# Optimization experiments

Hardware: AMD Instinct MI355X
Metric: run time of the kernel (lower is better)

## Reference

```python
import jax, jax.numpy as jnp
import numpy as np

B, T, E = 4, 2_000_000, 8
C, K, STRIDE = 128, 512, 512
CHUNK, OVERLAP = 64000, 511  # overlap defaults to kernel_size - 1


def _candidate_positions(T):
    """Exact set of window start positions visited by the chunked streaming max.

    Replays the chunk loop of _lowmem_max_over_time: chunk starts advance by
    step = chunk_size - overlap (not a multiple of stride!), and within each
    chunk conv windows start at chunk_start + stride*k.
    """
    step = max(1, CHUNK - OVERLAP)
    pos = []
    start = 0
    while start < T:
        end = min(start + CHUNK, T)
        end_ext = min(end + OVERLAP, T)
        L = end_ext - start
        if L >= K:
            n = (L - K) // STRIDE + 1
            pos.append(start + STRIDE * np.arange(n, dtype=np.int64))
        if end == T:
            break
        start += step
    p = np.unique(np.concatenate(pos))
    return np.clip(p, 0, max(0, T - K))


POS = _candidate_positions(T)                       # [P] static window starts
WIN_IDX = POS[:, None] + np.arange(K, dtype=np.int64)  # [P, K] gather indices


def setup_inputs() -> dict:
    key = jax.random.key(0)
    ks = jax.random.split(key, 5)
    scale = 1.0 / float(np.sqrt(E * K))  # torch Conv1d default init range
    return {
        "x": jax.random.normal(ks[0], (B, T, E), dtype=jnp.float32),
        "w1": jax.random.uniform(ks[1], (C, E, K), jnp.float32, -scale, scale),
        "b1": jax.random.uniform(ks[2], (C,), jnp.float32, -scale, scale),
        "w2": jax.random.uniform(ks[3], (C, E, K), jnp.float32, -scale, scale),
        "b2": jax.random.uniform(ks[4], (C,), jnp.float32, -scale, scale),
    }


def reference(x, w1, b1, w2, b2):
    # Gather every candidate window the chunked scan would see: [B, P, K, E]
    wins = x[:, WIN_IDX, :]
    # Original clones windows under no_grad (stop_grad_input=True): input gets no grad.
    wins = jax.lax.stop_gradient(wins)
    # Gated conv (GLU): conv1(z) * sigmoid(conv2(z)) at each window -> [B, C, P]
    c1 = jnp.einsum('bpke,cek->bcp', wins, w1) + b1[:, None]
    c2 = jnp.einsum('bpke,cek->bcp', wins, w2) + b2[:, None]
    g = c1 * jax.nn.sigmoid(c2)
    # Global max-over-time per (batch, channel); identical value to the
    # running-max pass followed by exact re-evaluation at argmax positions.
    return g.max(axis=-1)  # [B, C]
```

## Files before the change

### kernel.cpp

```cpp
#include <hip/hip_runtime.h>


#define T_LEN 2000000
#define P_CNT 3937
#define M_TOT 15748
#define KD    4096

typedef __attribute__((ext_vector_type(8))) short short8;
typedef __attribute__((ext_vector_type(4))) float f32x4;

static __device__ __forceinline__ unsigned short f2bf(float f) {
    unsigned u = __builtin_bit_cast(unsigned, f);
    unsigned r = (u + 0x7FFFu + ((u >> 16) & 1u)) >> 16;
    return (unsigned short)r;
}

static __device__ __forceinline__ unsigned ordenc(float f) {
    unsigned u = __builtin_bit_cast(unsigned, f);
    return (u & 0x80000000u) ? ~u : (u | 0x80000000u);
}

static __device__ __forceinline__ size_t row_base(int m) {
    if (m > M_TOT - 1) m = M_TOT - 1;
    int bb = m / P_CNT;
    int p  = m - bb * P_CNT;
    int j, kp;
    if (p < 3875) { j = p / 125; kp = p - j * 125; }
    else          { j = 31;      kp = p - 3875; }
    long pos = (long)j * 63489 + (long)kp * 512;
    return ((size_t)bb * T_LEN + (size_t)pos) * 8u;
}

static __device__ __forceinline__ uint2 cvt4(float4 v) {
    unsigned lo, hi;
    asm("v_cvt_pk_bf16_f32 %0, %1, %2" : "=v"(lo) : "v"(v.x), "v"(v.y));
    asm("v_cvt_pk_bf16_f32 %0, %1, %2" : "=v"(hi) : "v"(v.z), "v"(v.w));
    uint2 u; u.x = lo; u.y = hi;
    return u;
}

__global__ __launch_bounds__(256) void pack_w(const float* __restrict__ w1,
                                              const float* __restrict__ w2,
                                              uint4* __restrict__ Bpf,
                                              unsigned* __restrict__ outu) {
    int c = blockIdx.x * 256 + threadIdx.x;
    if (c < 512) outu[c] = 0u;
    if (c >= 131072) return;
    int l  = c & 63;
    int nt = (c >> 6) & 15;
    int kq = (c >> 10) & 1;
    int ks = c >> 11;
    int n  = nt * 16 + (l & 15);
    int kb = ks * 64 + kq * 32 + ((l >> 4) << 3);
    const float* src = (n < 128) ? w1 : w2;
    int cc = n & 127;
    unsigned short h[8];
#pragma unroll
    for (int j = 0; j < 8; ++j) {
        int k = kb + j;
        h[j] = f2bf(src[cc * 4096 + (k & 7) * 512 + (k >> 3)]);
    }
    uint4 v;
    v.x = (unsigned)h[0] | ((unsigned)h[1] << 16);
    v.y = (unsigned)h[2] | ((unsigned)h[3] << 16);
    v.z = (unsigned)h[4] | ((unsigned)h[5] << 16);
    v.w = (unsigned)h[6] | ((unsigned)h[7] << 16);
    Bpf[c] = v;
}

#define LOAD_B(BB, KS)                                                         \
    do {                                                                       \
        _Pragma("unroll")                                                      \
        for (int kq = 0; kq < 2; ++kq)                                         \
            _Pragma("unroll")                                                  \
            for (int nf = 0; nf < 2; ++nf)                                     \
                BB[kq][nf] = Bq[((KS) * 2 + kq) * 1024 + bbase + nf * 64];     \
    } while (0)

#define STEP(KS, BCUR, BNXT)                                                   \
    do {                                                                       \
        const int ks_ = (KS);                                                  \
        const int ksn = (ks_ + 1 < 64) ? ks_ + 1 : 63;                         \
        LOAD_B(BNXT, ksn);                                \
        const int ksl = (ks_ + 4 < 64) ? ks_ + 4 : 63;                         \
        float4 aF = *(const float4*)(x + aoff + (size_t)(ksl * 64));           \
        const char* As = smem + (ks_ & 3) * 4096;                              \
        _Pragma("unroll")                                                      \
        for (int kq = 0; kq < 2; ++kq) {                                       \
            short8 af0 = *(const short8*)(As + aro[kq][0]);                    \
            short8 af1 = *(const short8*)(As + aro[kq][1]);                    \
            short8 b0  = __builtin_bit_cast(short8, BCUR[kq][0]);              \
            short8 b1  = __builtin_bit_cast(short8, BCUR[kq][1]);              \
            acc[0][0] = __builtin_amdgcn_mfma_f32_16x16x32_bf16(               \
                af0, b0, acc[0][0], 0, 0, 0);                                  \
            acc[1][0] = __builtin_amdgcn_mfma_f32_16x16x32_bf16(               \
                af1, b0, acc[1][0], 0, 0, 0);                                  \
            acc[0][1] = __builtin_amdgcn_mfma_f32_16x16x32_bf16(               \
                af0, b1, acc[0][1], 0, 0, 0);                                  \
            acc[1][1] = __builtin_amdgcn_mfma_f32_16x16x32_bf16(               \
                af1, b1, acc[1][1], 0, 0, 0);                                  \
        }                                                                      \
                  \
        *(uint2*)(smem + ((ks_ + 2) & 3) * 4096 + awb) = cvt4(aA);             \
        aA = aB; aB = aF;                                                      \
        asm volatile("s_waitcnt lgkmcnt(0)" ::: "memory");                     \
        __builtin_amdgcn_s_barrier();                                          \
        asm volatile("" ::: "memory");                                         \
    } while (0)

__global__ __launch_bounds__(512, 4) void gemm_max(const float* __restrict__ x,
                                                   const uint4* __restrict__ Bq,
                                                   const float* __restrict__ b1,
                                                   const float* __restrict__ b2,
                                                   unsigned* __restrict__ outu) {
    __shared__ __align__(16) char smem[32768];

    const int t    = threadIdx.x;
    const int lane = t & 63;
    const int w    = t >> 6;
    const int m0   = blockIdx.x * 32;

    const int rowS = t >> 4;
    const int kcS  = t & 15;
    const size_t aoff = row_base(m0 + rowS) + (size_t)(kcS * 4);
    const int    awb  = (rowS * 128 + kcS * 8) ^ ((rowS & 7) << 4);

    int aro[2][2];
#pragma unroll
    for (int kq = 0; kq < 2; ++kq)
#pragma unroll
        for (int mf = 0; mf < 2; ++mf) {
            int row = mf * 16 + (lane & 15);
            aro[kq][mf] = (row * 128 + kq * 64 + (lane >> 4) * 16)
                          ^ ((row & 7) << 4);
        }

    const int bbase = w * 128 + lane;

#pragma unroll
    for (int pt = 0; pt < 2; ++pt) {
        float4 v = *(const float4*)(x + aoff + pt * 64);
        *(uint2*)(smem + pt * 4096 + awb) = cvt4(v);
    }
    __syncthreads();

    float4 aA = *(const float4*)(x + aoff + 128);
    float4 aB = *(const float4*)(x + aoff + 192);
    uint4 BX[2][2], BY[2][2];
    LOAD_B(BX, 0);

    f32x4 acc[2][2];
#pragma unroll
    for (int mf = 0; mf < 2; ++mf)
#pragma unroll
        for (int nf = 0; nf < 2; ++nf) acc[mf][nf] = (f32x4){0.f, 0.f, 0.f, 0.f};

    for (int ks = 0; ks < 64; ks += 2) {
        STEP(ks, BX, BY);
        STEP(ks + 1, BY, BX);
    }

    float* gt = (float*)smem;
#pragma unroll
    for (int mf = 0; mf < 2; ++mf)
#pragma unroll
        for (int nf = 0; nf < 2; ++nf) {
            int col = w * 32 + nf * 16 + (lane & 15);
#pragma unroll
            for (int q = 0; q < 4; ++q) {
                int row = mf * 16 + (lane >> 4) * 4 + q;
                gt[row * 256 + col] = acc[mf][nf][q];
            }
        }
    __syncthreads();

    if (t < 128) {
        const int   c   = t;
        const float bb1 = b1[c];
        const float bb2 = b2[c];
        int   bprev = (m0 < M_TOT ? m0 : M_TOT - 1) / P_CNT;
        float best  = -3.4e38f;
        for (int r = 0; r < 32; ++r) {
            int m = m0 + r;
            if (m > M_TOT - 1) m = M_TOT - 1;
            int bb = m / P_CNT;
            float c1 = gt[r * 256 + c] + bb1;
            float c2 = gt[r * 256 + 128 + c] + bb2;
            float g  = c1 / (1.f + __expf(-c2));
            if (bb != bprev) {
                atomicMax(&outu[bprev * 128 + c], ordenc(best));
                bprev = bb;
                best  = -3.4e38f;
            }
            best = fmaxf(best, g);
        }
        atomicMax(&outu[bprev * 128 + c], ordenc(best));
    }
}

__global__ __launch_bounds__(256) void unmap_out(unsigned* __restrict__ outu) {
    int i = blockIdx.x * 256 + threadIdx.x;
    if (i < 512) {
        unsigned u = outu[i];
        outu[i] = (u & 0x80000000u) ? (u ^ 0x80000000u) : ~u;
    }
}

extern "C" void kernel_launch(void* const* d_in, const int* in_sizes, int n_in,
                              void* d_out, int out_size, void* d_ws, size_t ws_size,
                              hipStream_t stream) {
    const float* x  = (const float*)d_in[0];
    const float* w1 = (const float*)d_in[1];
    const float* b1 = (const float*)d_in[2];
    const float* w2 = (const float*)d_in[3];
    const float* b2 = (const float*)d_in[4];

    uint4*    Bpf  = (uint4*)d_ws;
    unsigned* outu = (unsigned*)d_out;

    pack_w<<<dim3(512), dim3(256), 0, stream>>>(w1, w2, Bpf, outu);

    const int nblk = (M_TOT + 31) / 32;
    gemm_max<<<dim3(nblk), dim3(512), 0, stream>>>(x, (const uint4*)Bpf, b1, b2, outu);

    unmap_out<<<dim3(2), dim3(256), 0, stream>>>(outu);
}
```

Before: 81.92 us.

## Widen GEMM tile to 64 rows with 16 waves and fuse GLU-max into registers

Each block now covers 64 window rows of one batch using 1024 threads (16 waves). Weight columns are interleaved so every 16-wide MFMA tile holds 8 conv1 and 8 conv2 channels. The gated activation and the max are then computed in registers through lane shuffles, replacing the shared-memory staging and the serial 128-thread epilogue. Blocks are aligned to batch boundaries, so each channel needs a single atomic, and each wave loads half as much B per K step. The cost is a larger block, a 1024-thread launch bound that limits registers per thread, and only 248 blocks.

```diff
diff --git a/kernel.cpp b/kernel.cpp
--- a/kernel.cpp
+++ b/kernel.cpp
@@ -20,10 +20,7 @@
     return (u & 0x80000000u) ? ~u : (u | 0x80000000u);
 }
 
-static __device__ __forceinline__ size_t row_base(int m) {
-    if (m > M_TOT - 1) m = M_TOT - 1;
-    int bb = m / P_CNT;
-    int p  = m - bb * P_CNT;
+static __device__ __forceinline__ size_t row_base_bp(int bb, int p) {
     int j, kp;
     if (p < 3875) { j = p / 125; kp = p - j * 125; }
     else          { j = 31;      kp = p - 3875; }
@@ -47,10 +44,11 @@
     if (c < 512) outu[c] = 0u;
     if (c >= 131072) return;
     int l  = c & 63;
-    int nt = (c >> 6) & 15;
+    int w  = (c >> 6) & 15;
     int kq = (c >> 10) & 1;
     int ks = c >> 11;
-    int n  = nt * 16 + (l & 15);
+    int cl = l & 15;
+    int n  = (cl < 8) ? (w * 8 + cl) : (128 + w * 8 + (cl - 8));
     int kb = ks * 64 + kq * 32 + ((l >> 4) << 3);
     const float* src = (n < 128) ? w1 : w2;
     int cc = n & 127;
@@ -72,130 +70,106 @@
     do {                                                                       \
         _Pragma("unroll")                                                      \
         for (int kq = 0; kq < 2; ++kq)                                         \
-            _Pragma("unroll")                                                  \
-            for (int nf = 0; nf < 2; ++nf)                                     \
-                BB[kq][nf] = Bq[((KS) * 2 + kq) * 1024 + bbase + nf * 64];     \
+            BB[kq] = Bq[((KS) * 2 + kq) * 1024 + bbase];                       \
     } while (0)
 
 #define STEP(KS, BCUR, BNXT)                                                   \
     do {                                                                       \
         const int ks_ = (KS);                                                  \
         const int ksn = (ks_ + 1 < 64) ? ks_ + 1 : 63;                         \
-        LOAD_B(BNXT, ksn);                                \
+        LOAD_B(BNXT, ksn);                                                     \
         const int ksl = (ks_ + 4 < 64) ? ks_ + 4 : 63;                         \
         float4 aF = *(const float4*)(x + aoff + (size_t)(ksl * 64));           \
-        const char* As = smem + (ks_ & 3) * 4096;                              \
+        const char* As = smem + (ks_ & 3) * 8192;                              \
         _Pragma("unroll")                                                      \
         for (int kq = 0; kq < 2; ++kq) {                                       \
-            short8 af0 = *(const short8*)(As + aro[kq][0]);                    \
-            short8 af1 = *(const short8*)(As + aro[kq][1]);                    \
-            short8 b0  = __builtin_bit_cast(short8, BCUR[kq][0]);              \
-            short8 b1  = __builtin_bit_cast(short8, BCUR[kq][1]);              \
-            acc[0][0] = __builtin_amdgcn_mfma_f32_16x16x32_bf16(               \
-                af0, b0, acc[0][0], 0, 0, 0);                                  \
-            acc[1][0] = __builtin_amdgcn_mfma_f32_16x16x32_bf16(               \
-                af1, b0, acc[1][0], 0, 0, 0);                                  \
-            acc[0][1] = __builtin_amdgcn_mfma_f32_16x16x32_bf16(               \
-                af0, b1, acc[0][1], 0, 0, 0);                                  \
-            acc[1][1] = __builtin_amdgcn_mfma_f32_16x16x32_bf16(               \
-                af1, b1, acc[1][1], 0, 0, 0);                                  \
+            short8 b = __builtin_bit_cast(short8, BCUR[kq]);                   \
+            _Pragma("unroll")                                                  \
+            for (int mf = 0; mf < 4; ++mf) {                                   \
+                short8 af = *(const short8*)(As + aro[kq][mf]);                \
+                acc[mf] = __builtin_amdgcn_mfma_f32_16x16x32_bf16(             \
+                    af, b, acc[mf], 0, 0, 0);                                  \
+            }                                                                  \
         }                                                                      \
-                  \
-        *(uint2*)(smem + ((ks_ + 2) & 3) * 4096 + awb) = cvt4(aA);             \
+        *(uint2*)(smem + ((ks_ + 2) & 3) * 8192 + awb) = cvt4(aA);             \
         aA = aB; aB = aF;                                                      \
         asm volatile("s_waitcnt lgkmcnt(0)" ::: "memory");                     \
         __builtin_amdgcn_s_barrier();                                          \
         asm volatile("" ::: "memory");                                         \
     } while (0)
 
-__global__ __launch_bounds__(512, 4) void gemm_max(const float* __restrict__ x,
-                                                   const uint4* __restrict__ Bq,
-                                                   const float* __restrict__ b1,
-                                                   const float* __restrict__ b2,
-                                                   unsigned* __restrict__ outu) {
+__global__ __launch_bounds__(1024, 4) void gemm_max(const float* __restrict__ x,
+                                                    const uint4* __restrict__ Bq,
+                                                    const float* __restrict__ b1,
+                                                    const float* __restrict__ b2,
+                                                    unsigned* __restrict__ outu) {
     __shared__ __align__(16) char smem[32768];
 
     const int t    = threadIdx.x;
     const int lane = t & 63;
     const int w    = t >> 6;
-    const int m0   = blockIdx.x * 32;
+    const int bid  = blockIdx.x;
+    const int bb   = bid / 62;
+    const int p0   = (bid % 62) * 64;
 
     const int rowS = t >> 4;
     const int kcS  = t & 15;
-    const size_t aoff = row_base(m0 + rowS) + (size_t)(kcS * 4);
+    int pS = p0 + rowS; if (pS > P_CNT - 1) pS = P_CNT - 1;
+    const size_t aoff = row_base_bp(bb, pS) + (size_t)(kcS * 4);
     const int    awb  = (rowS * 128 + kcS * 8) ^ ((rowS & 7) << 4);
 
-    int aro[2][2];
+    int aro[2][2 * 2];
 #pragma unroll
     for (int kq = 0; kq < 2; ++kq)
 #pragma unroll
-        for (int mf = 0; mf < 2; ++mf) {
+        for (int mf = 0; mf < 4; ++mf) {
             int row = mf * 16 + (lane & 15);
             aro[kq][mf] = (row * 128 + kq * 64 + (lane >> 4) * 16)
                           ^ ((row & 7) << 4);
         }
 
-    const int bbase = w * 128 + lane;
+    const int bbase = w * 64 + lane;
 
 #pragma unroll
     for (int pt = 0; pt < 2; ++pt) {
         float4 v = *(const float4*)(x + aoff + pt * 64);
-        *(uint2*)(smem + pt * 4096 + awb) = cvt4(v);
+        *(uint2*)(smem + pt * 8192 + awb) = cvt4(v);
     }
     __syncthreads();
 
     float4 aA = *(const float4*)(x + aoff + 128);
     float4 aB = *(const float4*)(x + aoff + 192);
-    uint4 BX[2][2], BY[2][2];
+    uint4 BX[2], BY[2];
     LOAD_B(BX, 0);
 
-    f32x4 acc[2][2];
-#pragma unroll
-    for (int mf = 0; mf < 2; ++mf)
-#pragma unroll
-        for (int nf = 0; nf < 2; ++nf) acc[mf][nf] = (f32x4){0.f, 0.f, 0.f, 0.f};
+    f32x4 acc[4];
+#pragma unroll
+    for (int mf = 0; mf < 4; ++mf) acc[mf] = (f32x4){0.f, 0.f, 0.f, 0.f};
 
     for (int ks = 0; ks < 64; ks += 2) {
         STEP(ks, BX, BY);
         STEP(ks + 1, BY, BX);
     }
 
-    float* gt = (float*)smem;
-#pragma unroll
-    for (int mf = 0; mf < 2; ++mf)
-#pragma unroll
-        for (int nf = 0; nf < 2; ++nf) {
-            int col = w * 32 + nf * 16 + (lane & 15);
-#pragma unroll
-            for (int q = 0; q < 4; ++q) {
-                int row = mf * 16 + (lane >> 4) * 4 + q;
-                gt[row * 256 + col] = acc[mf][nf][q];
-            }
-        }
-    __syncthreads();
-
-    if (t < 128) {
-        const int   c   = t;
-        const float bb1 = b1[c];
-        const float bb2 = b2[c];
-        int   bprev = (m0 < M_TOT ? m0 : M_TOT - 1) / P_CNT;
-        float best  = -3.4e38f;
-        for (int r = 0; r < 32; ++r) {
-            int m = m0 + r;
-            if (m > M_TOT - 1) m = M_TOT - 1;
-            int bb = m / P_CNT;
-            float c1 = gt[r * 256 + c] + bb1;
-            float c2 = gt[r * 256 + 128 + c] + bb2;
+    const int   cidx = w * 8 + (lane & 7);
+    const float bb1  = b1[cidx];
+    const float bb2  = b2[cidx];
+    float best = -3.4e38f;
+#pragma unroll
+    for (int mf = 0; mf < 4; ++mf)
+#pragma unroll
+        for (int q = 0; q < 4; ++q) {
+            float v  = acc[mf][q];
+            float ov = __shfl_xor(v, 8);
+            float c1 = v + bb1;
+            float c2 = ov + bb2;
             float g  = c1 / (1.f + __expf(-c2));
-            if (bb != bprev) {
-                atomicMax(&outu[bprev * 128 + c], ordenc(best));
-                bprev = bb;
-                best  = -3.4e38f;
-            }
             best = fmaxf(best, g);
         }
-        atomicMax(&outu[bprev * 128 + c], ordenc(best));
-    }
+    best = fmaxf(best, __shfl_xor(best, 16));
+    best = fmaxf(best, __shfl_xor(best, 32));
+    if (lane < 8)
+        atomicMax(&outu[bb * 128 + w * 8 + lane], ordenc(best));
 }
 
 __global__ __launch_bounds__(256) void unmap_out(unsigned* __restrict__ outu) {
@@ -220,8 +194,8 @@
 
     pack_w<<<dim3(512), dim3(256), 0, stream>>>(w1, w2, Bpf, outu);
 
-    const int nblk = (M_TOT + 31) / 32;
-    gemm_max<<<dim3(nblk), dim3(512), 0, stream>>>(x, (const uint4*)Bpf, b1, b2, outu);
+    const int nblk = 62 * 4;
+    gemm_max<<<dim3(nblk), dim3(1024), 0, stream>>>(x, (const uint4*)Bpf, b1, b2, outu);
 
     unmap_out<<<dim3(2), dim3(256), 0, stream>>>(outu);
 }
```

Result: faster. 70.91 us (-13.4%).
